# Performance work log

Measured on AMD Instinct MI355X. Metric: run time of the kernel, lower is better.

The kernel has to match this reference:

```python
import jax, jax.numpy as jnp
import numpy as np

SCALE_CLS = 7.0
EPS = 1e-12

def _l2norm(x):
    # torch F.normalize: x / max(||x||_2, eps) along last dim
    n = jnp.sqrt(jnp.sum(x * x, axis=-1, keepdims=True))
    return x / jnp.maximum(n, EPS)

def setup_inputs() -> dict:
    key = jax.random.key(0)
    k1, k2 = jax.random.split(key)
    B, Q, C, D, H, W = 4, 75, 5, 512, 6, 6
    ftrain = jax.random.normal(k1, (B, Q, C, D, H, W), dtype=jnp.float32)
    ftest = jax.random.normal(k2, (B, Q, C, D, H, W), dtype=jnp.float32)
    return {"ftrain": ftrain, "ftest": ftest, "K": 28}

def reference(ftrain, ftest, K):
    B, Q, C, D, H, W = ftrain.shape
    P = H * W  # 36 spatial positions
    # spatial means -> [B,Q,C,1,D]
    ftest_mean = ftest.mean(axis=(4, 5))[:, :, :, None, :]
    ftrain_mean = ftrain.mean(axis=(4, 5))[:, :, :, None, :]
    # flatten spatial, move channel last -> [B,Q,C,P,D]
    ft = jnp.swapaxes(ftest.reshape(B, Q, C, D, P), 3, 4)
    fr = jnp.swapaxes(ftrain.reshape(B, Q, C, D, P), 3, 4)
    ft = _l2norm(ft)
    fr = _l2norm(fr)
    ftest_mean = _l2norm(ftest_mean)
    ftrain_mean = _l2norm(ftrain_mean)
    # global scores [B,Q,C]
    scores = SCALE_CLS * jnp.sum(jnp.squeeze(ftest_mean * ftrain_mean), axis=-1)
    # per-position scores [B,Q,C,P]
    ftrain_scores = SCALE_CLS * jnp.sum(ftest_mean * fr, axis=-1)
    ftest_scores = SCALE_CLS * jnp.sum(ft * ftrain_mean, axis=-1)
    # top-K positions (indices distinct, so one-hot-sum mask == gather)
    _, train_ind = jax.lax.top_k(ftrain_scores, K)  # [B,Q,C,K]
    _, test_ind = jax.lax.top_k(ftest_scores, K)
    # gather top-K spatial features and average -> [B,Q,C,D]
    ftest_fuse = jnp.take_along_axis(ft, test_ind[..., None], axis=3).sum(axis=3) / K
    ftrain_fuse = jnp.take_along_axis(fr, train_ind[..., None], axis=3).sum(axis=3) / K
    ftest_fuse = _l2norm(ftest_fuse)
    ftrain_fuse = _l2norm(ftrain_fuse)
    scores_final = SCALE_CLS * jnp.sum(ftest_fuse * ftrain_fuse, axis=-1)
    return (scores, scores_final)
```

## Files before the change

### kernel.cpp

```cpp
#include <hip/hip_runtime.h>
#include <hip/hip_fp16.h>
#include <stdint.h>

#define NGRP 1500
#define DD 512
#define PP 36
#define DP (DD*PP)
#define SWEEPS 19
#define SCALE_CLS 7.0f
#define EPS 1e-12f

__device__ __forceinline__ uint32_t packh2(float a, float b){
  __half2 h = __floats2half2_rn(a, b);
  union{__half2 h; uint32_t u;} z; z.h = h; return z.u;
}
__device__ __forceinline__ float2 unpackh2(uint32_t v){
  union{uint32_t u; __half2 h;} z; z.u = v;
  return __half22float2(z.h);
}
__device__ __forceinline__ float waveRed(float x){
  #pragma unroll
  for (int off = 32; off; off >>= 1) x += __shfl_xor(x, off, 64);
  return x;
}

__global__ __launch_bounds__(256, 2)
void topk_fuse(const float* __restrict__ gtrain,
               const float* __restrict__ gtest,
               const int* __restrict__ Kp,
               float* __restrict__ out)
{
  __shared__ float s_pt[252], s_pr[252];
  __shared__ float s_tm[28],  s_rm[28];
  __shared__ float s_q[PP], s_e[PP];
  __shared__ float s_a[PP], s_b[PP];
  __shared__ float s_st[PP], s_sr[PP];
  __shared__ float s_nt[PP], s_nr[PP];
  __shared__ float s_wt[PP], s_wr[PP];

  const int t    = threadIdx.x;
  const int lane = t & 63;
  const int wave = t >> 6;
  const int g    = blockIdx.x;
  const int K    = Kp[0];
  const int c    = t % 9;
  const int r    = t / 9;

  const float4* gt4 = (const float4*)(gtest  + (size_t)g * DP);
  const float4* gr4 = (const float4*)(gtrain + (size_t)g * DP);

  if (t < PP) { s_q[t] = 0.f; s_e[t] = 0.f; s_a[t] = 0.f; s_b[t] = 0.f; }

  uint32_t keepT[2*SWEEPS], keepR[2*SWEEPS];
  float4 q4 = {0,0,0,0}, e4 = {0,0,0,0}, a4 = {0,0,0,0}, b4 = {0,0,0,0};
  float pm2 = 0.f, pr2 = 0.f, pmr = 0.f;

  float4 T = {0,0,0,0}, R = {0,0,0,0};
  if (t < 252) { int i0 = r*9 + c; T = gt4[i0]; R = gr4[i0]; }

  #pragma unroll
  for (int k = 0; k < SWEEPS; ++k) {
    float4 Tn = {0,0,0,0}, Rn = {0,0,0,0};
    if (k < SWEEPS-1) {
      bool nact = (k+1 < SWEEPS-1) ? (t < 252) : (t < 72);
      if (nact) { int ni = (r + 28*(k+1))*9 + c; Tn = gt4[ni]; Rn = gr4[ni]; }
    }
    const bool cact = (k < SWEEPS-1) ? (t < 252) : (t < 72);

    if (cact) {
      s_pt[r*9 + c] = T.x + T.y + T.z + T.w;
      s_pr[r*9 + c] = R.x + R.y + R.z + R.w;
    }
    __syncthreads();

    const int rows = (k < SWEEPS-1) ? 28 : 8;
    if (t < rows) {
      float st = 0.f, sr = 0.f;
      #pragma unroll
      for (int j = 0; j < 9; ++j) { st += s_pt[t*9 + j]; sr += s_pr[t*9 + j]; }
      float tm = st * (1.0f/36.0f), rm = sr * (1.0f/36.0f);
      s_tm[t] = tm; s_rm[t] = rm;
      pm2 += tm*tm; pr2 += rm*rm; pmr += tm*rm;
    }
    __syncthreads();

    if (cact) {
      float tm = s_tm[r], rm = s_rm[r];
      q4.x += T.x*T.x; q4.y += T.y*T.y; q4.z += T.z*T.z; q4.w += T.w*T.w;
      e4.x += R.x*R.x; e4.y += R.y*R.y; e4.z += R.z*R.z; e4.w += R.w*R.w;
      a4.x += T.x*rm;  a4.y += T.y*rm;  a4.z += T.z*rm;  a4.w += T.w*rm;
      b4.x += R.x*tm;  b4.y += R.y*tm;  b4.z += R.z*tm;  b4.w += R.w*tm;
      keepT[2*k] = packh2(T.x, T.y); keepT[2*k+1] = packh2(T.z, T.w);
      keepR[2*k] = packh2(R.x, R.y); keepR[2*k+1] = packh2(R.z, R.w);
    } else {
      keepT[2*k] = 0u; keepT[2*k+1] = 0u; keepR[2*k] = 0u; keepR[2*k+1] = 0u;
    }
    T = Tn; R = Rn;
  }

  if (t < 252) {
    int p0 = c*4;
    atomicAdd(&s_q[p0+0], q4.x); atomicAdd(&s_q[p0+1], q4.y);
    atomicAdd(&s_q[p0+2], q4.z); atomicAdd(&s_q[p0+3], q4.w);
    atomicAdd(&s_e[p0+0], e4.x); atomicAdd(&s_e[p0+1], e4.y);
    atomicAdd(&s_e[p0+2], e4.z); atomicAdd(&s_e[p0+3], e4.w);
    atomicAdd(&s_a[p0+0], a4.x); atomicAdd(&s_a[p0+1], a4.y);
    atomicAdd(&s_a[p0+2], a4.z); atomicAdd(&s_a[p0+3], a4.w);
    atomicAdd(&s_b[p0+0], b4.x); atomicAdd(&s_b[p0+1], b4.y);
    atomicAdd(&s_b[p0+2], b4.z); atomicAdd(&s_b[p0+3], b4.w);
  }
  if (wave == 0) {
    float m2 = waveRed(pm2), r2 = waveRed(pr2), mr = waveRed(pmr);
    if (lane == 0) {
      float n1 = fmaxf(sqrtf(m2), EPS), n2 = fmaxf(sqrtf(r2), EPS);
      out[g] = SCALE_CLS * mr / (n1 * n2);
    }
  }
  __syncthreads();

  if (wave < 2 && lane < PP) {
    float q  = wave ? s_e[lane] : s_q[lane];
    float dm = wave ? s_b[lane] : s_a[lane];
    float n  = fmaxf(sqrtf(q), EPS);
    if (wave) { s_nr[lane] = n; s_sr[lane] = dm / n; }
    else      { s_nt[lane] = n; s_st[lane] = dm / n; }
  }
  __syncthreads();

  if (wave < 2 && lane < PP) {
    const float* sc = wave ? s_sr : s_st;
    const float* nn = wave ? s_nr : s_nt;
    float*       w  = wave ? s_wr : s_wt;
    float mine = sc[lane];
    int rank = 0;
    #pragma unroll
    for (int p = 0; p < PP; ++p) {
      float o = sc[p];
      rank += ((o > mine) || (o == mine && p < lane)) ? 1 : 0;
    }
    w[lane] = (rank < K) ? (1.0f / nn[lane]) : 0.f;
  }
  __syncthreads();

  float wt0=0,wt1=0,wt2=0,wt3=0, wr0=0,wr1=0,wr2=0,wr3=0;
  if (t < 252) {
    wt0 = s_wt[4*c+0]; wt1 = s_wt[4*c+1]; wt2 = s_wt[4*c+2]; wt3 = s_wt[4*c+3];
    wr0 = s_wr[4*c+0]; wr1 = s_wr[4*c+1]; wr2 = s_wr[4*c+2]; wr3 = s_wr[4*c+3];
  }
  float U2 = 0.f, V2 = 0.f, UV = 0.f;
  #pragma unroll
  for (int k = 0; k < SWEEPS; ++k) {
    const bool cact = (k < SWEEPS-1) ? (t < 252) : (t < 72);
    if (cact) {
      float2 t0 = unpackh2(keepT[2*k]), t1 = unpackh2(keepT[2*k+1]);
      float2 r0 = unpackh2(keepR[2*k]), r1 = unpackh2(keepR[2*k+1]);
      s_pt[r*9 + c] = t0.x*wt0 + t0.y*wt1 + t1.x*wt2 + t1.y*wt3;
      s_pr[r*9 + c] = r0.x*wr0 + r0.y*wr1 + r1.x*wr2 + r1.y*wr3;
    }
    __syncthreads();
    const int rows = (k < SWEEPS-1) ? 28 : 8;
    if (t < rows) {
      float u = 0.f, v = 0.f;
      #pragma unroll
      for (int j = 0; j < 9; ++j) { u += s_pt[t*9 + j]; v += s_pr[t*9 + j]; }
      U2 += u*u; V2 += v*v; UV += u*v;
    }
    __syncthreads();
  }
  if (wave == 0) {
    float u2 = waveRed(U2), v2 = waveRed(V2), uv = waveRed(UV);
    if (lane == 0) {
      float nu = fmaxf(sqrtf(u2), EPS), nv = fmaxf(sqrtf(v2), EPS);
      out[NGRP + g] = SCALE_CLS * uv / (nu * nv);
    }
  }
}

extern "C" void kernel_launch(void* const* d_in, const int* in_sizes, int n_in,
                              void* d_out, int out_size, void* d_ws, size_t ws_size,
                              hipStream_t stream)
{
  const float* ftrain = (const float*)d_in[0];
  const float* ftest  = (const float*)d_in[1];
  const int*   Kp     = (const int*)d_in[2];
  float*       out    = (float*)d_out;
  topk_fuse<<<NGRP, 256, 0, stream>>>(ftrain, ftest, Kp, out);
}
```

Before: 281.1 us.

## Issue all loads up front and reduce rows once via full shared buffers

Result: faster. 269.6 us (-4.1%).

```diff
diff --git a/kernel.cpp b/kernel.cpp
--- a/kernel.cpp
+++ b/kernel.cpp
@@ -1,5 +1,4 @@
 #include <hip/hip_runtime.h>
-#include <hip/hip_fp16.h>
 #include <stdint.h>
 
 #define NGRP 1500
@@ -10,14 +9,6 @@
 #define SCALE_CLS 7.0f
 #define EPS 1e-12f
 
-__device__ __forceinline__ uint32_t packh2(float a, float b){
-  __half2 h = __floats2half2_rn(a, b);
-  union{__half2 h; uint32_t u;} z; z.h = h; return z.u;
-}
-__device__ __forceinline__ float2 unpackh2(uint32_t v){
-  union{uint32_t u; __half2 h;} z; z.u = v;
-  return __half22float2(z.h);
-}
 __device__ __forceinline__ float waveRed(float x){
   #pragma unroll
   for (int off = 32; off; off >>= 1) x += __shfl_xor(x, off, 64);
@@ -30,13 +21,15 @@
                const int* __restrict__ Kp,
                float* __restrict__ out)
 {
-  __shared__ float s_pt[252], s_pr[252];
-  __shared__ float s_tm[28],  s_rm[28];
+  __shared__ float s_rt[DD*9];
+  __shared__ float s_rr[DD*9];
+  __shared__ float s_tm[DD], s_rm[DD];
   __shared__ float s_q[PP], s_e[PP];
   __shared__ float s_a[PP], s_b[PP];
   __shared__ float s_st[PP], s_sr[PP];
   __shared__ float s_nt[PP], s_nr[PP];
   __shared__ float s_wt[PP], s_wr[PP];
+  __shared__ float s_red[12];
 
   const int t    = threadIdx.x;
   const int lane = t & 63;
@@ -45,60 +38,62 @@
   const int K    = Kp[0];
   const int c    = t % 9;
   const int r    = t / 9;
+  const bool act = t < 252;
 
   const float4* gt4 = (const float4*)(gtest  + (size_t)g * DP);
   const float4* gr4 = (const float4*)(gtrain + (size_t)g * DP);
 
   if (t < PP) { s_q[t] = 0.f; s_e[t] = 0.f; s_a[t] = 0.f; s_b[t] = 0.f; }
 
-  uint32_t keepT[2*SWEEPS], keepR[2*SWEEPS];
-  float4 q4 = {0,0,0,0}, e4 = {0,0,0,0}, a4 = {0,0,0,0}, b4 = {0,0,0,0};
-  float pm2 = 0.f, pr2 = 0.f, pmr = 0.f;
-
-  float4 T = {0,0,0,0}, R = {0,0,0,0};
-  if (t < 252) { int i0 = r*9 + c; T = gt4[i0]; R = gr4[i0]; }
-
+  float4 keepT[SWEEPS], keepR[SWEEPS];
+  float4 q4 = {0,0,0,0}, e4 = {0,0,0,0};
   #pragma unroll
   for (int k = 0; k < SWEEPS; ++k) {
-    float4 Tn = {0,0,0,0}, Rn = {0,0,0,0};
-    if (k < SWEEPS-1) {
-      bool nact = (k+1 < SWEEPS-1) ? (t < 252) : (t < 72);
-      if (nact) { int ni = (r + 28*(k+1))*9 + c; Tn = gt4[ni]; Rn = gr4[ni]; }
+    const bool cact = (k < SWEEPS-1) ? act : (t < 72);
+    float4 T = {0,0,0,0}, R = {0,0,0,0};
+    if (cact) { int i = t + 252*k; T = gt4[i]; R = gr4[i]; }
+    keepT[k] = T; keepR[k] = R;
+    q4.x += T.x*T.x; q4.y += T.y*T.y; q4.z += T.z*T.z; q4.w += T.w*T.w;
+    e4.x += R.x*R.x; e4.y += R.y*R.y; e4.z += R.z*R.z; e4.w += R.w*R.w;
+    if (cact) {
+      s_rt[t + 252*k] = T.x + T.y + T.z + T.w;
+      s_rr[t + 252*k] = R.x + R.y + R.z + R.w;
     }
-    const bool cact = (k < SWEEPS-1) ? (t < 252) : (t < 72);
+  }
+  __syncthreads();
 
-    if (cact) {
-      s_pt[r*9 + c] = T.x + T.y + T.z + T.w;
-      s_pr[r*9 + c] = R.x + R.y + R.z + R.w;
-    }
-    __syncthreads();
-
-    const int rows = (k < SWEEPS-1) ? 28 : 8;
-    if (t < rows) {
-      float st = 0.f, sr = 0.f;
-      #pragma unroll
-      for (int j = 0; j < 9; ++j) { st += s_pt[t*9 + j]; sr += s_pr[t*9 + j]; }
-      float tm = st * (1.0f/36.0f), rm = sr * (1.0f/36.0f);
-      s_tm[t] = tm; s_rm[t] = rm;
-      pm2 += tm*tm; pr2 += rm*rm; pmr += tm*rm;
-    }
-    __syncthreads();
-
-    if (cact) {
-      float tm = s_tm[r], rm = s_rm[r];
-      q4.x += T.x*T.x; q4.y += T.y*T.y; q4.z += T.z*T.z; q4.w += T.w*T.w;
-      e4.x += R.x*R.x; e4.y += R.y*R.y; e4.z += R.z*R.z; e4.w += R.w*R.w;
-      a4.x += T.x*rm;  a4.y += T.y*rm;  a4.z += T.z*rm;  a4.w += T.w*rm;
-      b4.x += R.x*tm;  b4.y += R.y*tm;  b4.z += R.z*tm;  b4.w += R.w*tm;
-      keepT[2*k] = packh2(T.x, T.y); keepT[2*k+1] = packh2(T.z, T.w);
-      keepR[2*k] = packh2(R.x, R.y); keepR[2*k+1] = packh2(R.z, R.w);
-    } else {
-      keepT[2*k] = 0u; keepT[2*k+1] = 0u; keepR[2*k] = 0u; keepR[2*k+1] = 0u;
-    }
-    T = Tn; R = Rn;
+  float pm2 = 0.f, pr2 = 0.f, pmr = 0.f;
+  #pragma unroll
+  for (int h = 0; h < 2; ++h) {
+    int d = t + 256*h;
+    float st = 0.f, sr = 0.f;
+    #pragma unroll
+    for (int j = 0; j < 9; ++j) { st += s_rt[d*9 + j]; sr += s_rr[d*9 + j]; }
+    float tm = st * (1.0f/36.0f), rm = sr * (1.0f/36.0f);
+    s_tm[d] = tm; s_rm[d] = rm;
+    pm2 += tm*tm; pr2 += rm*rm; pmr += tm*rm;
+  }
+  pm2 = waveRed(pm2); pr2 = waveRed(pr2); pmr = waveRed(pmr);
+  if (lane == 0) { s_red[wave] = pm2; s_red[4+wave] = pr2; s_red[8+wave] = pmr; }
+  __syncthreads();
+  if (t == 0) {
+    float m2 = s_red[0]+s_red[1]+s_red[2]+s_red[3];
+    float r2 = s_red[4]+s_red[5]+s_red[6]+s_red[7];
+    float mr = s_red[8]+s_red[9]+s_red[10]+s_red[11];
+    float n1 = fmaxf(sqrtf(m2), EPS), n2 = fmaxf(sqrtf(r2), EPS);
+    out[g] = SCALE_CLS * mr / (n1 * n2);
   }
 
-  if (t < 252) {
+  float4 a4 = {0,0,0,0}, b4 = {0,0,0,0};
+  #pragma unroll
+  for (int k = 0; k < SWEEPS; ++k) {
+    int d = r + 28*k; if (d > 511) d = 511;
+    float tm = s_tm[d], rm = s_rm[d];
+    float4 T = keepT[k], R = keepR[k];
+    a4.x += T.x*rm; a4.y += T.y*rm; a4.z += T.z*rm; a4.w += T.w*rm;
+    b4.x += R.x*tm; b4.y += R.y*tm; b4.z += R.z*tm; b4.w += R.w*tm;
+  }
+  if (act) {
     int p0 = c*4;
     atomicAdd(&s_q[p0+0], q4.x); atomicAdd(&s_q[p0+1], q4.y);
     atomicAdd(&s_q[p0+2], q4.z); atomicAdd(&s_q[p0+3], q4.w);
@@ -108,13 +103,6 @@
     atomicAdd(&s_a[p0+2], a4.z); atomicAdd(&s_a[p0+3], a4.w);
     atomicAdd(&s_b[p0+0], b4.x); atomicAdd(&s_b[p0+1], b4.y);
     atomicAdd(&s_b[p0+2], b4.z); atomicAdd(&s_b[p0+3], b4.w);
-  }
-  if (wave == 0) {
-    float m2 = waveRed(pm2), r2 = waveRed(pr2), mr = waveRed(pmr);
-    if (lane == 0) {
-      float n1 = fmaxf(sqrtf(m2), EPS), n2 = fmaxf(sqrtf(r2), EPS);
-      out[g] = SCALE_CLS * mr / (n1 * n2);
-    }
   }
   __syncthreads();
 
@@ -143,36 +131,38 @@
   __syncthreads();
 
   float wt0=0,wt1=0,wt2=0,wt3=0, wr0=0,wr1=0,wr2=0,wr3=0;
-  if (t < 252) {
+  if (act) {
     wt0 = s_wt[4*c+0]; wt1 = s_wt[4*c+1]; wt2 = s_wt[4*c+2]; wt3 = s_wt[4*c+3];
     wr0 = s_wr[4*c+0]; wr1 = s_wr[4*c+1]; wr2 = s_wr[4*c+2]; wr3 = s_wr[4*c+3];
   }
+  #pragma unroll
+  for (int k = 0; k < SWEEPS; ++k) {
+    const bool cact = (k < SWEEPS-1) ? act : (t < 72);
+    if (cact) {
+      float4 T = keepT[k], R = keepR[k];
+      s_rt[t + 252*k] = T.x*wt0 + T.y*wt1 + T.z*wt2 + T.w*wt3;
+      s_rr[t + 252*k] = R.x*wr0 + R.y*wr1 + R.z*wr2 + R.w*wr3;
+    }
+  }
+  __syncthreads();
   float U2 = 0.f, V2 = 0.f, UV = 0.f;
   #pragma unroll
-  for (int k = 0; k < SWEEPS; ++k) {
-    const bool cact = (k < SWEEPS-1) ? (t < 252) : (t < 72);
-    if (cact) {
-      float2 t0 = unpackh2(keepT[2*k]), t1 = unpackh2(keepT[2*k+1]);
-      float2 r0 = unpackh2(keepR[2*k]), r1 = unpackh2(keepR[2*k+1]);
-      s_pt[r*9 + c] = t0.x*wt0 + t0.y*wt1 + t1.x*wt2 + t1.y*wt3;
-      s_pr[r*9 + c] = r0.x*wr0 + r0.y*wr1 + r1.x*wr2 + r1.y*wr3;
-    }
-    __syncthreads();
-    const int rows = (k < SWEEPS-1) ? 28 : 8;
-    if (t < rows) {
-      float u = 0.f, v = 0.f;
-      #pragma unroll
-      for (int j = 0; j < 9; ++j) { u += s_pt[t*9 + j]; v += s_pr[t*9 + j]; }
-      U2 += u*u; V2 += v*v; UV += u*v;
-    }
-    __syncthreads();
+  for (int h = 0; h < 2; ++h) {
+    int d = t + 256*h;
+    float u = 0.f, v = 0.f;
+    #pragma unroll
+    for (int j = 0; j < 9; ++j) { u += s_rt[d*9 + j]; v += s_rr[d*9 + j]; }
+    U2 += u*u; V2 += v*v; UV += u*v;
   }
-  if (wave == 0) {
-    float u2 = waveRed(U2), v2 = waveRed(V2), uv = waveRed(UV);
-    if (lane == 0) {
-      float nu = fmaxf(sqrtf(u2), EPS), nv = fmaxf(sqrtf(v2), EPS);
-      out[NGRP + g] = SCALE_CLS * uv / (nu * nv);
-    }
+  U2 = waveRed(U2); V2 = waveRed(V2); UV = waveRed(UV);
+  if (lane == 0) { s_red[wave] = U2; s_red[4+wave] = V2; s_red[8+wave] = UV; }
+  __syncthreads();
+  if (t == 0) {
+    float u2 = s_red[0]+s_red[1]+s_red[2]+s_red[3];
+    float v2 = s_red[4]+s_red[5]+s_red[6]+s_red[7];
+    float uv = s_red[8]+s_red[9]+s_red[10]+s_red[11];
+    float nu = fmaxf(sqrtf(u2), EPS), nv = fmaxf(sqrtf(v2), EPS);
+    out[NGRP + g] = SCALE_CLS * uv / (nu * nv);
   }
 }
 
```
